# Kernel optimization log

Hardware: AMD Instinct MI355X
Metric: run time of the kernel (lower is better)

The kernel has to match this reference:

```python
import jax, jax.numpy as jnp
import numpy as np

HIDDEN = 2048
N_HEADS = 16
HEAD_DIM = HIDDEN // N_HEADS
ROPE_BASE = 10000.0


def rotate_half(x):
    half = x.shape[-1] // 2
    return jnp.concatenate((-x[..., half:], x[..., :half]), axis=-1)


def rope_cos_sin(seq_len, dtype):
    inv_freq = 1.0 / (ROPE_BASE ** (jnp.arange(0, HEAD_DIM, 2, dtype=jnp.float32) / HEAD_DIM))
    pos = jnp.arange(seq_len, dtype=jnp.float32)
    freqs = jnp.einsum('i,j->ij', pos, inv_freq)  # [S, hd/2]
    emb = jnp.concatenate((freqs, freqs), axis=-1)  # [S, hd]
    return jnp.cos(emb).astype(dtype), jnp.sin(emb).astype(dtype)


def setup_inputs() -> dict:
    key = jax.random.key(0)
    ks = jax.random.split(key, 9)
    B, S, H = 2, 2048, HIDDEN
    std = 1.0 / np.sqrt(H)
    return {
        'hidden_states': jax.random.normal(ks[0], (B, S, H), dtype=jnp.float32),
        'Wq': jax.random.uniform(ks[1], (H, H), jnp.float32, -std, std),
        'bq': jax.random.uniform(ks[2], (H,), jnp.float32, -std, std),
        'Wk': jax.random.uniform(ks[3], (H, H), jnp.float32, -std, std),
        'bk': jax.random.uniform(ks[4], (H,), jnp.float32, -std, std),
        'Wv': jax.random.uniform(ks[5], (H, H), jnp.float32, -std, std),
        'bv': jax.random.uniform(ks[6], (H,), jnp.float32, -std, std),
        'Wo': jax.random.uniform(ks[7], (H, H), jnp.float32, -std, std),
        'bo': jax.random.uniform(ks[8], (H,), jnp.float32, -std, std),
    }


def reference(hidden_states, Wq, bq, Wk, bk, Wv, bv, Wo, bo):
    B, S, H = hidden_states.shape
    scale = HEAD_DIM ** -0.5

    def proj(W, b):
        # torch Linear: x @ W.T + b
        y = jnp.einsum('bsh,oh->bso', hidden_states, W) + b
        return y.reshape(B, S, N_HEADS, HEAD_DIM).transpose(0, 2, 1, 3)  # [B,nh,S,hd]

    q = proj(Wq, bq)
    k = proj(Wk, bk)
    v = proj(Wv, bv)

    cos, sin = rope_cos_sin(S, hidden_states.dtype)  # [S, hd]
    cos = cos[None, None, :, :]
    sin = sin[None, None, :, :]
    q = q * cos + rotate_half(q) * sin
    k = k * cos + rotate_half(k) * sin

    scores = jnp.einsum('bhqd,bhkd->bhqk', q, k) * scale  # [B,nh,S,S]
    probs = jax.nn.softmax(scores, axis=-1)
    ctx = jnp.einsum('bhqk,bhkd->bhqd', probs, v)
    ctx = ctx.transpose(0, 2, 1, 3).reshape(B, S, H)
    return jnp.einsum('bsh,oh->bso', ctx, Wo) + bo
```

## Files before the change

### kernel.cpp

```cpp
#include <hip/hip_runtime.h>
#include <hip/hip_bf16.h>
#include <math.h>

#define HIDDEN 2048
#define NH 16
#define HD 128
#define NB 2
#define SEQ 2048
#define K_DIM 2048

typedef unsigned int u32;
typedef unsigned short ushort_t;
typedef __bf16 bf16x8 __attribute__((ext_vector_type(8)));
typedef float f32x4 __attribute__((ext_vector_type(4)));
typedef ushort_t u16x8 __attribute__((ext_vector_type(8)));

__device__ __forceinline__ void split1(float x, unsigned short& h, unsigned short& l) {
    u32 u = __float_as_uint(x);
    u32 hr = (u + 0x7FFFu + ((u >> 16) & 1u)) >> 16;
    h = (unsigned short)hr;
    float r = x - __uint_as_float(hr << 16);
    u32 u2 = __float_as_uint(r);
    l = (unsigned short)((u2 + 0x7FFFu + ((u2 >> 16) & 1u)) >> 16);
}

__device__ __forceinline__ ushort_t bf16r(float x) {
    u32 u = __float_as_uint(x);
    return (ushort_t)((u + 0x7FFFu + ((u >> 16) & 1u)) >> 16);
}

__device__ __forceinline__ void gl_lds16(const void* g, void* l) {
    __builtin_amdgcn_global_load_lds(
        (const __attribute__((address_space(1))) u32*)g,
        (__attribute__((address_space(3))) u32*)l, 16, 0, 0);
}

__global__ void k_rope_tables(float* __restrict__ ct, float* __restrict__ st) {
    int idx = blockIdx.x * 256 + threadIdx.x;
    int s = idx >> 6, d = idx & 63;
    double inv = pow(10000.0, -(double)d * (1.0 / 64.0));
    double ang = (double)s * inv;
    ct[idx] = (float)cos(ang);
    st[idx] = (float)sin(ang);
}

#define XG 2097152
#define WG 1048576
__global__ void k_cvt_all(const float4* __restrict__ X, const float4* __restrict__ W0,
                          const float4* __restrict__ W1, const float4* __restrict__ W2,
                          ushort4* __restrict__ Xh, ushort4* __restrict__ H0,
                          ushort4* __restrict__ H1, ushort4* __restrict__ H2) {
    int idx = blockIdx.x * 256 + threadIdx.x;
    const float4* src;
    ushort4* dst;
    int off;
    if (idx < XG) { src = X; dst = Xh; off = idx; }
    else {
        int t = idx - XG;
        int m = t >> 20;
        off = t & (WG - 1);
        src = (m == 0) ? W0 : (m == 1) ? W1 : W2;
        dst = (m == 0) ? H0 : (m == 1) ? H1 : H2;
    }
    float4 x = src[off];
    ushort4 h;
    h.x = bf16r(x.x); h.y = bf16r(x.y); h.z = bf16r(x.z); h.w = bf16r(x.w);
    dst[off] = h;
}

__global__ void k_split(const float4* __restrict__ src, ushort4* __restrict__ hi,
                        ushort4* __restrict__ lo) {
    int idx = blockIdx.x * 256 + threadIdx.x;
    float4 x = src[idx];
    ushort4 h, l;
    split1(x.x, h.x, l.x);
    split1(x.y, h.y, l.y);
    split1(x.z, h.z, l.z);
    split1(x.w, h.w, l.w);
    hi[idx] = h;
    lo[idx] = l;
}

__global__ __launch_bounds__(256)
void k_gemm_qkv(const ushort_t* __restrict__ Xh,
                const ushort_t* __restrict__ W0, const ushort_t* __restrict__ W1,
                const ushort_t* __restrict__ W2,
                const float* __restrict__ b0, const float* __restrict__ b1,
                const float* __restrict__ b2,
                float* __restrict__ o0, float* __restrict__ o1, float* __restrict__ o2) {
    __shared__ ushort_t As[128 * 32];
    __shared__ ushort_t Bs[128 * 32];
    const int tid = threadIdx.x;
    const int lane = tid & 63;
    const int w = tid >> 6;
    const int wm = w & 1, wn = w >> 1;
    const int quad = lane >> 4;
    const int l15 = lane & 15;
    const int m0 = blockIdx.x << 7;
    const int mat = blockIdx.y >> 4;
    const int n0 = (blockIdx.y & 15) << 7;
    const ushort_t* Wsel = (mat == 0) ? W0 : (mat == 1) ? W1 : W2;
    const float* bias = (mat == 0) ? b0 : (mat == 1) ? b1 : b2;
    float* out = (mat == 0) ? o0 : (mat == 1) ? o1 : o2;

    const ushort_t* src = (w < 2) ? Xh : Wsel;
    const int rbase = ((w < 2) ? m0 : n0) + (w & 1) * 64;
    ushort_t* lbase = ((w < 2) ? As : Bs) + (w & 1) * 64 * 32;
    const int lrow = lane >> 2;
    const int lk = (lane & 3) << 3;
    const ushort_t* gp[4];
    ushort_t* lp[4];
#pragma unroll
    for (int i = 0; i < 4; i++) {
        gp[i] = src + (size_t)(rbase + i * 16 + lrow) * K_DIM + lk;
        lp[i] = lbase + i * 512;
    }

    f32x4 acc[4][4];
#pragma unroll
    for (int i = 0; i < 4; i++)
#pragma unroll
        for (int j = 0; j < 4; j++) acc[i][j] = (f32x4){0.f, 0.f, 0.f, 0.f};

    const int aoff = (wm * 64 + l15) * 32 + quad * 8;
    const int boff = (wn * 64 + l15) * 32 + quad * 8;

#pragma unroll
    for (int i = 0; i < 4; i++) gl_lds16(gp[i], lp[i]);
    __syncthreads();
    bf16x8 ah[4], bh[4];
#pragma unroll
    for (int f = 0; f < 4; f++) {
        ah[f] = *(const bf16x8*)&As[aoff + f * 512];
        bh[f] = *(const bf16x8*)&Bs[boff + f * 512];
    }

    for (int kt = 32; kt <= K_DIM; kt += 32) {
        __syncthreads();
        if (kt < K_DIM) {
#pragma unroll
            for (int i = 0; i < 4; i++) gl_lds16(gp[i] + kt, lp[i]);
        }
#pragma unroll
        for (int fm = 0; fm < 4; fm++)
#pragma unroll
            for (int fn = 0; fn < 4; fn++)
                acc[fm][fn] = __builtin_amdgcn_mfma_f32_16x16x32_bf16(ah[fm], bh[fn], acc[fm][fn], 0, 0, 0);
        if (kt < K_DIM) {
            __syncthreads();
#pragma unroll
            for (int f = 0; f < 4; f++) {
                ah[f] = *(const bf16x8*)&As[aoff + f * 512];
                bh[f] = *(const bf16x8*)&Bs[boff + f * 512];
            }
        }
    }

    float bcolv[4];
#pragma unroll
    for (int fn = 0; fn < 4; fn++) bcolv[fn] = bias[n0 + wn * 64 + fn * 16 + l15];

    const int h = n0 >> 7;
    const int bb = m0 >> 11;
    const int sb = (m0 & (SEQ - 1)) + wm * 64 + quad * 4;
    const int d = wn * 64 + l15;
    float* obase = out + ((size_t)(bb * NH + h) * SEQ) * HD;
#pragma unroll
    for (int fm = 0; fm < 4; fm++)
#pragma unroll
        for (int fn = 0; fn < 4; fn++)
#pragma unroll
            for (int r = 0; r < 4; r++)
                obase[(size_t)(sb + fm * 16 + r) * HD + d + fn * 16] =
                    acc[fm][fn][r] + bcolv[fn];
}

__global__ __launch_bounds__(256)
void k_gemm_mfma(const ushort_t* __restrict__ Ah, const ushort_t* __restrict__ Al,
                 const ushort_t* __restrict__ Bh, const ushort_t* __restrict__ Bl,
                 const float* __restrict__ bias, float* __restrict__ out) {
    __shared__ ushort_t lds[4][128 * 32];
    const int tid = threadIdx.x;
    const int lane = tid & 63;
    const int w = tid >> 6;
    const int wm = w & 1, wn = w >> 1;
    const int quad = lane >> 4;
    const int l15 = lane & 15;
    const int m0 = blockIdx.x << 7;
    const int n0 = blockIdx.y << 7;

    const ushort_t* src = (w == 0) ? Ah : (w == 1) ? Al : (w == 2) ? Bh : Bl;
    const int rbase = (w < 2) ? m0 : n0;
    const int lrow = lane >> 2;
    const int lk = (lane & 3) << 3;
    const ushort_t* gp[8];
    ushort_t* lp[8];
#pragma unroll
    for (int i = 0; i < 8; i++) {
        gp[i] = src + (size_t)(rbase + i * 16 + lrow) * K_DIM + lk;
        lp[i] = &lds[w][i * 512];
    }

    f32x4 acc[4][4];
#pragma unroll
    for (int i = 0; i < 4; i++)
#pragma unroll
        for (int j = 0; j < 4; j++) acc[i][j] = (f32x4){0.f, 0.f, 0.f, 0.f};

    const int aoff = (wm * 64 + l15) * 32 + quad * 8;
    const int boff = (wn * 64 + l15) * 32 + quad * 8;

#pragma unroll
    for (int i = 0; i < 8; i++) gl_lds16(gp[i], lp[i]);
    __syncthreads();
    bf16x8 ah[4], al[4], bh[4], bl[4];
#pragma unroll
    for (int f = 0; f < 4; f++) {
        ah[f] = *(const bf16x8*)&lds[0][aoff + f * 512];
        al[f] = *(const bf16x8*)&lds[1][aoff + f * 512];
        bh[f] = *(const bf16x8*)&lds[2][boff + f * 512];
        bl[f] = *(const bf16x8*)&lds[3][boff + f * 512];
    }

    for (int kt = 32; kt <= K_DIM; kt += 32) {
        __syncthreads();
        if (kt < K_DIM) {
#pragma unroll
            for (int i = 0; i < 8; i++) gl_lds16(gp[i] + kt, lp[i]);
        }
#pragma unroll
        for (int fm = 0; fm < 4; fm++)
#pragma unroll
            for (int fn = 0; fn < 4; fn++) {
                acc[fm][fn] = __builtin_amdgcn_mfma_f32_16x16x32_bf16(ah[fm], bh[fn], acc[fm][fn], 0, 0, 0);
                acc[fm][fn] = __builtin_amdgcn_mfma_f32_16x16x32_bf16(ah[fm], bl[fn], acc[fm][fn], 0, 0, 0);
                acc[fm][fn] = __builtin_amdgcn_mfma_f32_16x16x32_bf16(al[fm], bh[fn], acc[fm][fn], 0, 0, 0);
            }
        if (kt < K_DIM) {
            __syncthreads();
#pragma unroll
            for (int f = 0; f < 4; f++) {
                ah[f] = *(const bf16x8*)&lds[0][aoff + f * 512];
                al[f] = *(const bf16x8*)&lds[1][aoff + f * 512];
                bh[f] = *(const bf16x8*)&lds[2][boff + f * 512];
                bl[f] = *(const bf16x8*)&lds[3][boff + f * 512];
            }
        }
    }

    float bcolv[4];
#pragma unroll
    for (int fn = 0; fn < 4; fn++) bcolv[fn] = bias[n0 + wn * 64 + fn * 16 + l15];

    const int mb = m0 + wm * 64 + quad * 4;
    const int nb = n0 + wn * 64 + l15;
#pragma unroll
    for (int fm = 0; fm < 4; fm++)
#pragma unroll
        for (int fn = 0; fn < 4; fn++)
#pragma unroll
            for (int r = 0; r < 4; r++)
                out[(size_t)(mb + fm * 16 + r) * HIDDEN + nb + fn * 16] =
                    acc[fm][fn][r] + bcolv[fn];
}

__global__ void k_rope_pack(const float* __restrict__ q, const float* __restrict__ k,
                            const float* __restrict__ ct, const float* __restrict__ st,
                            ushort_t* __restrict__ Qb, ushort_t* __restrict__ Kb) {
    int idx = blockIdx.x * 256 + threadIdx.x;
    int d = idx & 63;
    int s = (idx >> 6) & (SEQ - 1);
    int bh = idx >> 17;
    size_t base = ((size_t)bh * SEQ + s) * HD;
    float c = ct[(s << 6) + d], sn = st[(s << 6) + d];
    const float scq = 0.08838834764831845f;
    float q0 = q[base + d], q1 = q[base + d + 64];
    Qb[base + d]      = bf16r((q0 * c - q1 * sn) * scq);
    Qb[base + d + 64] = bf16r((q1 * c + q0 * sn) * scq);
    float k0 = k[base + d], k1 = k[base + d + 64];
    Kb[base + d]      = bf16r(k0 * c - k1 * sn);
    Kb[base + d + 64] = bf16r(k1 * c + k0 * sn);
}

__global__ __launch_bounds__(256)
void k_vpack(const float* __restrict__ v, ushort_t* __restrict__ vt) {
    __shared__ float t[64][65];
    const int tid = threadIdx.x;
    const int bh = blockIdx.z;
    const int s0 = blockIdx.x << 6;
    const int d0 = blockIdx.y << 6;
    const float* src = v + ((size_t)bh * SEQ + s0) * HD + d0;
    const int rr = tid >> 4;
    const int cc = (tid & 15) << 2;
#pragma unroll
    for (int i = 0; i < 4; i++) {
        float4 x = *(const float4*)(src + (size_t)(i * 16 + rr) * HD + cc);
        t[i * 16 + rr][cc] = x.x;
        t[i * 16 + rr][cc + 1] = x.y;
        t[i * 16 + rr][cc + 2] = x.z;
        t[i * 16 + rr][cc + 3] = x.w;
    }
    __syncthreads();
    const int dr = tid >> 2;
    const int sc_ = (tid & 3) << 4;
    ushort_t* dst = vt + ((size_t)bh * HD + d0 + dr) * SEQ + s0 + sc_;
    u16x8 o0, o1;
#pragma unroll
    for (int u = 0; u < 8; u++) o0[u] = bf16r(t[sc_ + u][dr]);
#pragma unroll
    for (int u = 0; u < 8; u++) o1[u] = bf16r(t[sc_ + 8 + u][dr]);
    *(u16x8*)dst = o0;
    *(u16x8*)(dst + 8) = o1;
}

__global__ __launch_bounds__(256, 2)
void k_flash_mfma(const ushort_t* __restrict__ Qb, const ushort_t* __restrict__ Kb,
                  const ushort_t* __restrict__ Vt,
                  ushort_t* __restrict__ ch, ushort_t* __restrict__ cl) {
    __shared__ ushort_t KV[128 * 136];
    __shared__ ushort_t Ps[128 * 136];
    const int tid = threadIdx.x;
    const int lane = tid & 63;
    const int w = tid >> 6;
    const int quad = lane >> 4;
    const int l15 = lane & 15;
    const int qt = blockIdx.x, h = blockIdx.y, b = blockIdx.z;
    const size_t bh = (size_t)(b * NH + h);
    const ushort_t* Qg = Qb + (bh * SEQ + ((size_t)qt << 7)) * HD;
    const ushort_t* Kg = Kb + bh * SEQ * HD;
    const ushort_t* Vg = Vt + bh * HD * SEQ;

    bf16x8 qf[2][4];
#pragma unroll
    for (int qi = 0; qi < 2; qi++)
#pragma unroll
        for (int ks = 0; ks < 4; ks++)
            qf[qi][ks] = *(const bf16x8*)(Qg + (size_t)(w * 32 + qi * 16 + l15) * HD + ks * 32 + quad * 8);

    const int sr = tid >> 4;
    const int sc8 = (tid & 15) << 3;

    u16x8 Kreg[8], Vreg[8];
#pragma unroll
    for (int i = 0; i < 8; i++)
        Kreg[i] = *(const u16x8*)(Kg + (size_t)(i * 16 + sr) * HD + sc8);
#pragma unroll
    for (int i = 0; i < 8; i++)
        Vreg[i] = *(const u16x8*)(Vg + (size_t)(i * 16 + sr) * SEQ + sc8);

    f32x4 acc[2][8];
#pragma unroll
    for (int qi = 0; qi < 2; qi++)
#pragma unroll
        for (int d = 0; d < 8; d++) acc[qi][d] = (f32x4){0.f, 0.f, 0.f, 0.f};
    float lp[2] = {0.f, 0.f};

    for (int kt = 0; kt < SEQ; kt += 128) {
        const int np = kt + 128;
        __syncthreads();
#pragma unroll
        for (int i = 0; i < 8; i++)
            *(u16x8*)&KV[(i * 16 + sr) * 136 + sc8] = Kreg[i];
        if (np < SEQ) {
#pragma unroll
            for (int i = 0; i < 8; i++)
                Kreg[i] = *(const u16x8*)(Kg + (size_t)(np + i * 16 + sr) * HD + sc8);
        }
        __syncthreads();

        f32x4 sc[2][8];
#pragma unroll
        for (int qi = 0; qi < 2; qi++)
#pragma unroll
            for (int j = 0; j < 8; j++) sc[qi][j] = (f32x4){0.f, 0.f, 0.f, 0.f};
#pragma unroll
        for (int ks = 0; ks < 4; ks++) {
#pragma unroll
            for (int jh = 0; jh < 2; jh++) {
                bf16x8 kf[4];
#pragma unroll
                for (int j = 0; j < 4; j++)
                    kf[j] = *(const bf16x8*)&KV[((jh * 4 + j) * 16 + l15) * 136 + ks * 32 + quad * 8];
#pragma unroll
                for (int qi = 0; qi < 2; qi++)
#pragma unroll
                    for (int j = 0; j < 4; j++)
                        sc[qi][jh * 4 + j] = __builtin_amdgcn_mfma_f32_16x16x32_bf16(
                            kf[j], qf[qi][ks], sc[qi][jh * 4 + j], 0, 0, 0);
            }
        }

#pragma unroll
        for (int qi = 0; qi < 2; qi++) {
            const int prow = (w * 32 + qi * 16 + l15) * 136 + quad * 4;
#pragma unroll
            for (int j = 0; j < 8; j++) {
                float p0 = __expf(sc[qi][j][0]);
                float p1 = __expf(sc[qi][j][1]);
                float p2 = __expf(sc[qi][j][2]);
                float p3 = __expf(sc[qi][j][3]);
                lp[qi] += (p0 + p1) + (p2 + p3);
                __hip_bfloat162 lo2 = __float22bfloat162_rn({p0, p1});
                __hip_bfloat162 hi2 = __float22bfloat162_rn({p2, p3});
                uint2 pk = make_uint2(*(u32*)&lo2, *(u32*)&hi2);
                *(uint2*)&Ps[prow + j * 16] = pk;
            }
        }
        __syncthreads();
#pragma unroll
        for (int i = 0; i < 8; i++)
            *(u16x8*)&KV[(i * 16 + sr) * 136 + sc8] = Vreg[i];
        if (np < SEQ) {
#pragma unroll
            for (int i = 0; i < 8; i++)
                Vreg[i] = *(const u16x8*)(Vg + (size_t)(i * 16 + sr) * SEQ + np + sc8);
        }
        __syncthreads();

#pragma unroll
        for (int ks = 0; ks < 4; ks++) {
            bf16x8 pf[2];
#pragma unroll
            for (int qi = 0; qi < 2; qi++)
                pf[qi] = *(const bf16x8*)&Ps[(w * 32 + qi * 16 + l15) * 136 + ks * 32 + quad * 8];
#pragma unroll
            for (int db = 0; db < 8; db++) {
                bf16x8 vf = *(const bf16x8*)&KV[(db * 16 + l15) * 136 + ks * 32 + quad * 8];
#pragma unroll
                for (int qi = 0; qi < 2; qi++)
                    acc[qi][db] = __builtin_amdgcn_mfma_f32_16x16x32_bf16(vf, pf[qi], acc[qi][db], 0, 0, 0);
            }
        }
    }

#pragma unroll
    for (int qi = 0; qi < 2; qi++) {
        lp[qi] += __shfl_xor(lp[qi], 16);
        lp[qi] += __shfl_xor(lp[qi], 32);
        float inv = 1.0f / lp[qi];
        int s = (qt << 7) + w * 32 + qi * 16 + l15;
        size_t base = ((size_t)b * SEQ + s) * HIDDEN + (h << 7) + quad * 4;
#pragma unroll
        for (int db = 0; db < 8; db++) {
            ushort4 hh, ll;
            split1(acc[qi][db][0] * inv, hh.x, ll.x);
            split1(acc[qi][db][1] * inv, hh.y, ll.y);
            split1(acc[qi][db][2] * inv, hh.z, ll.z);
            split1(acc[qi][db][3] * inv, hh.w, ll.w);
            *(ushort4*)&ch[base + db * 16] = hh;
            *(ushort4*)&cl[base + db * 16] = ll;
        }
    }
}

extern "C" void kernel_launch(void* const* d_in, const int* in_sizes, int n_in,
                              void* d_out, int out_size, void* d_ws, size_t ws_size,
                              hipStream_t stream) {
    const float* X  = (const float*)d_in[0];
    const float* Wq = (const float*)d_in[1];
    const float* bq = (const float*)d_in[2];
    const float* Wk = (const float*)d_in[3];
    const float* bk = (const float*)d_in[4];
    const float* Wv = (const float*)d_in[5];
    const float* bv = (const float*)d_in[6];
    const float* Wo = (const float*)d_in[7];
    const float* bo = (const float*)d_in[8];
    float* out = (float*)d_out;

    const size_t QS = (size_t)NB * NH * SEQ * HD;
    const size_t WS = (size_t)HIDDEN * HIDDEN;
    float* q_ws = (float*)d_ws;
    float* k_ws = q_ws + QS;
    float* v_ws = k_ws + QS;
    float* cost = v_ws + QS;
    float* sint = cost + (size_t)SEQ * 64;
    ushort_t* Xh = (ushort_t*)(sint + (size_t)SEQ * 64);
    ushort_t* Wh0 = Xh + QS;
    ushort_t* Wh1 = Wh0 + WS;
    ushort_t* Wh2 = Wh1 + WS;
    ushort_t* Woh = Wh2 + WS;
    ushort_t* Wol = Woh + WS;
    ushort_t* Kb  = Wol + WS;
    ushort_t* Vtb = Kb + QS;
    ushort_t* ctxh = (ushort_t*)q_ws;
    ushort_t* ctxl = ctxh + QS;

    k_rope_tables<<<(SEQ * 64) / 256, 256, 0, stream>>>(cost, sint);

    k_cvt_all<<<(XG + 3 * WG) / 256, 256, 0, stream>>>(
        (const float4*)X, (const float4*)Wq, (const float4*)Wk, (const float4*)Wv,
        (ushort4*)Xh, (ushort4*)Wh0, (ushort4*)Wh1, (ushort4*)Wh2);
    k_split<<<WS / 4 / 256, 256, 0, stream>>>((const float4*)Wo, (ushort4*)Woh, (ushort4*)Wol);

    k_gemm_qkv<<<dim3(32, 48), 256, 0, stream>>>(Xh, Wh0, Wh1, Wh2, bq, bk, bv,
                                                 q_ws, k_ws, v_ws);

    ushort_t* Qbb = Xh;
    k_rope_pack<<<(NB * NH * SEQ * 64) / 256, 256, 0, stream>>>(q_ws, k_ws, cost, sint, Qbb, Kb);
    k_vpack<<<dim3(SEQ / 64, HD / 64, NB * NH), 256, 0, stream>>>(v_ws, Vtb);

    k_flash_mfma<<<dim3(SEQ / 128, NH, NB), 256, 0, stream>>>(Qbb, Kb, Vtb, ctxh, ctxl);

    k_gemm_mfma<<<dim3(32, 16), 256, 0, stream>>>(ctxh, ctxl, Woh, Wol, bo, out);
}
```

Baseline: 540.5 us.

## Enlarge flash query tile to 256 rows and stage context output through LDS

```diff
diff --git a/kernel.cpp b/kernel.cpp
--- a/kernel.cpp
+++ b/kernel.cpp
@@ -176,9 +176,9 @@
 }
 
 __global__ __launch_bounds__(256)
-void k_gemm_mfma(const ushort_t* __restrict__ Ah, const ushort_t* __restrict__ Al,
-                 const ushort_t* __restrict__ Bh, const ushort_t* __restrict__ Bl,
-                 const float* __restrict__ bias, float* __restrict__ out) {
+void k_gemm_o(const ushort_t* __restrict__ Ah, const ushort_t* __restrict__ Al,
+              const ushort_t* __restrict__ Bh, const ushort_t* __restrict__ Bl,
+              const float* __restrict__ bias, float* __restrict__ out) {
     __shared__ ushort_t lds[4][128 * 32];
     const int tid = threadIdx.x;
     const int lane = tid & 63;
@@ -188,16 +188,22 @@
     const int l15 = lane & 15;
     const int m0 = blockIdx.x << 7;
     const int n0 = blockIdx.y << 7;
+    const bool isA = (w < 2);
 
     const ushort_t* src = (w == 0) ? Ah : (w == 1) ? Al : (w == 2) ? Bh : Bl;
-    const int rbase = (w < 2) ? m0 : n0;
     const int lrow = lane >> 2;
     const int lk = (lane & 3) << 3;
     const ushort_t* gp[8];
     ushort_t* lp[8];
 #pragma unroll
     for (int i = 0; i < 8; i++) {
-        gp[i] = src + (size_t)(rbase + i * 16 + lrow) * K_DIM + lk;
+        if (isA) {
+            int m = m0 + i * 16 + lrow;
+            int bb = m >> 11, s = m & (SEQ - 1);
+            gp[i] = src + ((size_t)bb * NH * SEQ + s) * HD + lk;
+        } else {
+            gp[i] = src + (size_t)(n0 + i * 16 + lrow) * K_DIM + lk;
+        }
         lp[i] = &lds[w][i * 512];
     }
 
@@ -225,8 +231,9 @@
     for (int kt = 32; kt <= K_DIM; kt += 32) {
         __syncthreads();
         if (kt < K_DIM) {
-#pragma unroll
-            for (int i = 0; i < 8; i++) gl_lds16(gp[i] + kt, lp[i]);
+            const size_t koff = isA ? ((size_t)(kt >> 7) * (SEQ * HD) + (kt & 127)) : (size_t)kt;
+#pragma unroll
+            for (int i = 0; i < 8; i++) gl_lds16(gp[i] + koff, lp[i]);
         }
 #pragma unroll
         for (int fm = 0; fm < 4; fm++)
@@ -313,29 +320,30 @@
     *(u16x8*)(dst + 8) = o1;
 }
 
-__global__ __launch_bounds__(256, 2)
+__global__ __launch_bounds__(256, 1)
 void k_flash_mfma(const ushort_t* __restrict__ Qb, const ushort_t* __restrict__ Kb,
                   const ushort_t* __restrict__ Vt,
                   ushort_t* __restrict__ ch, ushort_t* __restrict__ cl) {
     __shared__ ushort_t KV[128 * 136];
-    __shared__ ushort_t Ps[128 * 136];
+    __shared__ ushort_t Ps[256 * 136];
     const int tid = threadIdx.x;
     const int lane = tid & 63;
     const int w = tid >> 6;
     const int quad = lane >> 4;
     const int l15 = lane & 15;
-    const int qt = blockIdx.x, h = blockIdx.y, b = blockIdx.z;
-    const size_t bh = (size_t)(b * NH + h);
-    const ushort_t* Qg = Qb + (bh * SEQ + ((size_t)qt << 7)) * HD;
-    const ushort_t* Kg = Kb + bh * SEQ * HD;
-    const ushort_t* Vg = Vt + bh * HD * SEQ;
-
-    bf16x8 qf[2][4];
-#pragma unroll
-    for (int qi = 0; qi < 2; qi++)
+    const int bi = blockIdx.x;
+    const int bh = bi & 31;
+    const int qt = bi >> 5;
+    const ushort_t* Qg = Qb + ((size_t)bh * SEQ + ((size_t)qt << 8)) * HD;
+    const ushort_t* Kg = Kb + (size_t)bh * SEQ * HD;
+    const ushort_t* Vg = Vt + (size_t)bh * HD * SEQ;
+
+    bf16x8 qf[4][4];
+#pragma unroll
+    for (int qi = 0; qi < 4; qi++)
 #pragma unroll
         for (int ks = 0; ks < 4; ks++)
-            qf[qi][ks] = *(const bf16x8*)(Qg + (size_t)(w * 32 + qi * 16 + l15) * HD + ks * 32 + quad * 8);
+            qf[qi][ks] = *(const bf16x8*)(Qg + (size_t)(w * 64 + qi * 16 + l15) * HD + ks * 32 + quad * 8);
 
     const int sr = tid >> 4;
     const int sc8 = (tid & 15) << 3;
@@ -348,12 +356,12 @@
     for (int i = 0; i < 8; i++)
         Vreg[i] = *(const u16x8*)(Vg + (size_t)(i * 16 + sr) * SEQ + sc8);
 
-    f32x4 acc[2][8];
-#pragma unroll
-    for (int qi = 0; qi < 2; qi++)
+    f32x4 acc[4][8];
+#pragma unroll
+    for (int qi = 0; qi < 4; qi++)
 #pragma unroll
         for (int d = 0; d < 8; d++) acc[qi][d] = (f32x4){0.f, 0.f, 0.f, 0.f};
-    float lp[2] = {0.f, 0.f};
+    float lsum[4] = {0.f, 0.f, 0.f, 0.f};
 
     for (int kt = 0; kt < SEQ; kt += 128) {
         const int np = kt + 128;
@@ -368,38 +376,35 @@
         }
         __syncthreads();
 
-        f32x4 sc[2][8];
-#pragma unroll
-        for (int qi = 0; qi < 2; qi++)
+        f32x4 sc[4][8];
+#pragma unroll
+        for (int qi = 0; qi < 4; qi++)
 #pragma unroll
             for (int j = 0; j < 8; j++) sc[qi][j] = (f32x4){0.f, 0.f, 0.f, 0.f};
 #pragma unroll
         for (int ks = 0; ks < 4; ks++) {
-#pragma unroll
-            for (int jh = 0; jh < 2; jh++) {
-                bf16x8 kf[4];
-#pragma unroll
-                for (int j = 0; j < 4; j++)
-                    kf[j] = *(const bf16x8*)&KV[((jh * 4 + j) * 16 + l15) * 136 + ks * 32 + quad * 8];
-#pragma unroll
-                for (int qi = 0; qi < 2; qi++)
-#pragma unroll
-                    for (int j = 0; j < 4; j++)
-                        sc[qi][jh * 4 + j] = __builtin_amdgcn_mfma_f32_16x16x32_bf16(
-                            kf[j], qf[qi][ks], sc[qi][jh * 4 + j], 0, 0, 0);
-            }
-        }
-
-#pragma unroll
-        for (int qi = 0; qi < 2; qi++) {
-            const int prow = (w * 32 + qi * 16 + l15) * 136 + quad * 4;
+            bf16x8 kf[8];
+#pragma unroll
+            for (int j = 0; j < 8; j++)
+                kf[j] = *(const bf16x8*)&KV[(j * 16 + l15) * 136 + ks * 32 + quad * 8];
+#pragma unroll
+            for (int qi = 0; qi < 4; qi++)
+#pragma unroll
+                for (int j = 0; j < 8; j++)
+                    sc[qi][j] = __builtin_amdgcn_mfma_f32_16x16x32_bf16(
+                        kf[j], qf[qi][ks], sc[qi][j], 0, 0, 0);
+        }
+
+#pragma unroll
+        for (int qi = 0; qi < 4; qi++) {
+            const int prow = (w * 64 + qi * 16 + l15) * 136 + quad * 4;
 #pragma unroll
             for (int j = 0; j < 8; j++) {
                 float p0 = __expf(sc[qi][j][0]);
                 float p1 = __expf(sc[qi][j][1]);
                 float p2 = __expf(sc[qi][j][2]);
                 float p3 = __expf(sc[qi][j][3]);
-                lp[qi] += (p0 + p1) + (p2 + p3);
+                lsum[qi] += (p0 + p1) + (p2 + p3);
                 __hip_bfloat162 lo2 = __float22bfloat162_rn({p0, p1});
                 __hip_bfloat162 hi2 = __float22bfloat162_rn({p2, p3});
                 uint2 pk = make_uint2(*(u32*)&lo2, *(u32*)&hi2);
@@ -419,37 +424,69 @@
 
 #pragma unroll
         for (int ks = 0; ks < 4; ks++) {
-            bf16x8 pf[2];
-#pragma unroll
-            for (int qi = 0; qi < 2; qi++)
-                pf[qi] = *(const bf16x8*)&Ps[(w * 32 + qi * 16 + l15) * 136 + ks * 32 + quad * 8];
+            bf16x8 pf[4];
+#pragma unroll
+            for (int qi = 0; qi < 4; qi++)
+                pf[qi] = *(const bf16x8*)&Ps[(w * 64 + qi * 16 + l15) * 136 + ks * 32 + quad * 8];
 #pragma unroll
             for (int db = 0; db < 8; db++) {
                 bf16x8 vf = *(const bf16x8*)&KV[(db * 16 + l15) * 136 + ks * 32 + quad * 8];
 #pragma unroll
-                for (int qi = 0; qi < 2; qi++)
+                for (int qi = 0; qi < 4; qi++)
                     acc[qi][db] = __builtin_amdgcn_mfma_f32_16x16x32_bf16(vf, pf[qi], acc[qi][db], 0, 0, 0);
             }
         }
     }
 
-#pragma unroll
-    for (int qi = 0; qi < 2; qi++) {
-        lp[qi] += __shfl_xor(lp[qi], 16);
-        lp[qi] += __shfl_xor(lp[qi], 32);
-        float inv = 1.0f / lp[qi];
-        int s = (qt << 7) + w * 32 + qi * 16 + l15;
-        size_t base = ((size_t)b * SEQ + s) * HIDDEN + (h << 7) + quad * 4;
+    float inv[4];
+#pragma unroll
+    for (int qi = 0; qi < 4; qi++) {
+        float l = lsum[qi];
+        l += __shfl_xor(l, 16);
+        l += __shfl_xor(l, 32);
+        inv[qi] = 1.0f / l;
+    }
+    const size_t obase = ((size_t)bh * SEQ + ((size_t)qt << 8)) * HD;
+
+    __syncthreads();
+#pragma unroll
+    for (int qi = 0; qi < 4; qi++)
 #pragma unroll
         for (int db = 0; db < 8; db++) {
-            ushort4 hh, ll;
-            split1(acc[qi][db][0] * inv, hh.x, ll.x);
-            split1(acc[qi][db][1] * inv, hh.y, ll.y);
-            split1(acc[qi][db][2] * inv, hh.z, ll.z);
-            split1(acc[qi][db][3] * inv, hh.w, ll.w);
-            *(ushort4*)&ch[base + db * 16] = hh;
-            *(ushort4*)&cl[base + db * 16] = ll;
-        }
+            ushort4 hh;
+            ushort_t dum;
+            split1(acc[qi][db][0] * inv[qi], hh.x, dum);
+            split1(acc[qi][db][1] * inv[qi], hh.y, dum);
+            split1(acc[qi][db][2] * inv[qi], hh.z, dum);
+            split1(acc[qi][db][3] * inv[qi], hh.w, dum);
+            *(ushort4*)&Ps[(w * 64 + qi * 16 + l15) * 136 + db * 16 + quad * 4] = hh;
+        }
+    __syncthreads();
+#pragma unroll
+    for (int t = 0; t < 16; t++) {
+        int c = t * 256 + tid;
+        int row = c >> 4, col8 = (c & 15) << 3;
+        *(u16x8*)&ch[obase + (size_t)row * HD + col8] = *(const u16x8*)&Ps[row * 136 + col8];
+    }
+    __syncthreads();
+#pragma unroll
+    for (int qi = 0; qi < 4; qi++)
+#pragma unroll
+        for (int db = 0; db < 8; db++) {
+            ushort4 ll;
+            ushort_t dum;
+            split1(acc[qi][db][0] * inv[qi], dum, ll.x);
+            split1(acc[qi][db][1] * inv[qi], dum, ll.y);
+            split1(acc[qi][db][2] * inv[qi], dum, ll.z);
+            split1(acc[qi][db][3] * inv[qi], dum, ll.w);
+            *(ushort4*)&Ps[(w * 64 + qi * 16 + l15) * 136 + db * 16 + quad * 4] = ll;
+        }
+    __syncthreads();
+#pragma unroll
+    for (int t = 0; t < 16; t++) {
+        int c = t * 256 + tid;
+        int row = c >> 4, col8 = (c & 15) << 3;
+        *(u16x8*)&cl[obase + (size_t)row * HD + col8] = *(const u16x8*)&Ps[row * 136 + col8];
     }
 }
 
@@ -499,7 +536,7 @@
     k_rope_pack<<<(NB * NH * SEQ * 64) / 256, 256, 0, stream>>>(q_ws, k_ws, cost, sint, Qbb, Kb);
     k_vpack<<<dim3(SEQ / 64, HD / 64, NB * NH), 256, 0, stream>>>(v_ws, Vtb);
 
-    k_flash_mfma<<<dim3(SEQ / 128, NH, NB), 256, 0, stream>>>(Qbb, Kb, Vtb, ctxh, ctxl);
-
-    k_gemm_mfma<<<dim3(32, 16), 256, 0, stream>>>(ctxh, ctxl, Woh, Wol, bo, out);
-}
+    k_flash_mfma<<<256, 256, 0, stream>>>(Qbb, Kb, Vtb, ctxh, ctxl);
+
+    k_gemm_o<<<dim3(32, 16), 256, 0, stream>>>(ctxh, ctxl, Woh, Wol, bo, out);
+}
```

Measured after the change: 599.1 us. +10.8%, slower.
